# Performance work log

Measured on AMD Instinct MI355X. Metric: run time of the kernel, lower is better.

The kernel has to match this reference:

```python
import jax, jax.numpy as jnp
import numpy as np
import math

L, DIN, DZ, H, C, NQ, NP = 768, 384, 128, 12, 16, 4, 6
C_SQU = 1.0 / math.sqrt(C)            # scalar qk scale
W_C = math.sqrt(2.0 / (9 * NQ))       # point-distance scale


def _w(key, fan_in, fan_out):
    return jax.random.normal(key, (fan_in, fan_out), dtype=jnp.float32) / math.sqrt(fan_in)


def setup_inputs() -> dict:
    key = jax.random.key(0)
    ks = jax.random.split(key, 20)
    inp = {
        "s": jax.random.normal(ks[0], (L, DIN), dtype=jnp.float32),
        "z": jax.random.normal(ks[1], (L, L, DZ), dtype=jnp.float32),
        "rot": jax.random.normal(ks[2], (L, 3, 3), dtype=jnp.float32),
        "trans": jax.random.normal(ks[3], (L, 3), dtype=jnp.float32),
        "Wq1": _w(ks[4], DIN, H * C),
        "Wk1": _w(ks[5], DIN, H * C),
        "Wv1": _w(ks[6], DIN, H * C),
        "Wq2": _w(ks[7], DIN, H * NQ * 3),
        "Wk2": _w(ks[8], DIN, H * NQ * 3),
        "Wv3": _w(ks[9], DIN, H * NP * 3),
        "Wz": _w(ks[10], DZ, H),
        "W1": _w(ks[11], H * DZ, DIN),
        "b1": jnp.zeros((DIN,), dtype=jnp.float32),
        "W2": _w(ks[12], H * C, DIN),
        "b2": jnp.zeros((DIN,), dtype=jnp.float32),
        "W3": _w(ks[13], H * NP * 3, DIN),
        "b3": jnp.zeros((DIN,), dtype=jnp.float32),
        "gamma": jnp.zeros((H,), dtype=jnp.float32),
    }
    return inp


def ipa_transform(x, rot, trans):
    # x: [L,H,P,3] local points -> global: rot @ x + trans
    return jnp.einsum('lij,lhpj->lhpi', rot, x) + trans[:, None, None, :]


def ipa_inverse_transform(x, rot, trans):
    # global -> local: rot^T @ (x - trans)
    return jnp.einsum('lji,lhpj->lhpi', rot, x - trans[:, None, None, :])


def reference(s, z, rot, trans, Wq1, Wk1, Wv1, Wq2, Wk2, Wv3, Wz,
              W1, b1, W2, b2, W3, b3, gamma):
    q1 = (s @ Wq1).reshape(L, H, C)
    k1 = (s @ Wk1).reshape(L, H, C)
    v1 = (s @ Wv1).reshape(L, H, C)
    att = jnp.einsum('ihc,jhc->ijh', q1, k1) * C_SQU          # [L,L,H]
    bias_z = z @ Wz                                           # [L,L,H]
    q2 = ipa_transform((s @ Wq2).reshape(L, H, NQ, 3), rot, trans)
    k2 = ipa_transform((s @ Wk2).reshape(L, H, NQ, 3), rot, trans)
    # squared-distance map sum over query points & xyz, via |q|^2+|k|^2-2qk
    sq = jnp.sum(q2 * q2, axis=(-2, -1))                      # [L,H]
    sk = jnp.sum(k2 * k2, axis=(-2, -1))                      # [L,H]
    cross = jnp.einsum('ihqt,jhqt->ijh', q2, k2)              # [L,L,H]
    dismap = sq[:, None, :] + sk[None, :, :] - 2.0 * cross
    # NOTE: no softmax in the original module — raw scores weight the values.
    att = att + bias_z - jax.nn.softplus(gamma)[None, None, :] * dismap * (W_C * 0.5)
    o1 = jnp.einsum('ijh,ijd->ihd', att, z)                   # [L,H,DZ]
    o2 = jnp.einsum('jhc,ijh->ihc', v1, att)                  # [L,H,C]
    v3 = ipa_transform((s @ Wv3).reshape(L, H, NP, 3), rot, trans)
    o3 = ipa_inverse_transform(jnp.einsum('jhpt,ijh->ihpt', v3, att), rot, trans)
    out = (o1.reshape(L, -1) @ W1 + b1) \
        + (o2.reshape(L, -1) @ W2 + b2) \
        + (o3.reshape(L, -1) @ W3 + b3)
    return out
```

## Files before the change

### kernel.cpp

```cpp
#include <hip/hip_runtime.h>
#include <math.h>
#include <stdint.h>

#define LL 768
#define DIN 384
#define HH 12
#define NLIN 1080
#define WC_HALF 0.11785113019775792f
#define C_SQU 0.25f

#define OFF_LIN    0u
#define OFF_VT     829440u
#define OFF_QBH    1050624u
#define OFF_QBL    1198080u
#define OFF_KBH    1345536u
#define OFF_KBL    1492992u
#define OFF_WZ     1640448u
#define OFF_SQWH   1641472u
#define OFF_SKWH   1650688u
#define OFF_SX     1659904u
#define OFF_O2     8737792u
#define OFF_O3     8885248u
#define OFF_PO1    9051136u

typedef __attribute__((ext_vector_type(8))) short short8v;
typedef __attribute__((ext_vector_type(4))) float float4v;

__device__ __forceinline__ ushort f2bu(float f) {
    union { float f; uint32_t u; } v; v.f = f;
    uint32_t r = (v.u + 0x7FFFu + ((v.u >> 16) & 1u)) >> 16;
    return (ushort)r;
}
__device__ __forceinline__ float bu2f(ushort u) {
    union { uint32_t u; float f; } v; v.u = ((uint32_t)u) << 16; return v.f;
}
__device__ __forceinline__ int fswz(int j) {
    return (((j >> 3) << 1) | ((j >> 1) & 1)) << 4;
}

__global__ __launch_bounds__(256) void gemm_lin_kernel(
    const float* __restrict__ s,
    const float* __restrict__ Wq1, const float* __restrict__ Wk1,
    const float* __restrict__ Wv1, const float* __restrict__ Wq2,
    const float* __restrict__ Wk2, const float* __restrict__ Wv3,
    float* __restrict__ lin)
{
    const int n0 = blockIdx.x * 64;
    const int i0 = blockIdx.y * 64;
    const int tid = threadIdx.x;
    __shared__ float sT[64][17];
    __shared__ float wT[16][65];
    const int tc = tid & 15, tr = tid >> 4;
    float acc[4][4] = {};
    for (int k0 = 0; k0 < DIN; k0 += 16) {
        __syncthreads();
        for (int idx = tid; idx < 1024; idx += 256) {
            int r = idx >> 4, kk = idx & 15;
            sT[r][kk] = s[(size_t)(i0 + r) * DIN + k0 + kk];
        }
        for (int idx = tid; idx < 1024; idx += 256) {
            int kk = idx >> 6, c = idx & 63;
            int col = n0 + c;
            float v = 0.f;
            if (col < NLIN) {
                const float* W; int nout, cc2;
                if      (col < 192) { W = Wq1; nout = 192; cc2 = col; }
                else if (col < 384) { W = Wk1; nout = 192; cc2 = col - 192; }
                else if (col < 576) { W = Wv1; nout = 192; cc2 = col - 384; }
                else if (col < 720) { W = Wq2; nout = 144; cc2 = col - 576; }
                else if (col < 864) { W = Wk2; nout = 144; cc2 = col - 720; }
                else                { W = Wv3; nout = 216; cc2 = col - 864; }
                v = W[(size_t)(k0 + kk) * nout + cc2];
            }
            wT[kk][c] = v;
        }
        __syncthreads();
        #pragma unroll
        for (int kk = 0; kk < 16; ++kk) {
            float a[4], b[4];
            #pragma unroll
            for (int r = 0; r < 4; ++r) a[r] = sT[tr * 4 + r][kk];
            #pragma unroll
            for (int c = 0; c < 4; ++c) b[c] = wT[kk][tc * 4 + c];
            #pragma unroll
            for (int r = 0; r < 4; ++r)
                #pragma unroll
                for (int c = 0; c < 4; ++c) acc[r][c] += a[r] * b[c];
        }
    }
    for (int r = 0; r < 4; ++r)
        for (int c = 0; c < 4; ++c) {
            int col = n0 + tc * 4 + c;
            if (col < NLIN)
                lin[(size_t)(i0 + tr * 4 + r) * NLIN + col] = acc[r][c];
        }
}

__global__ __launch_bounds__(192) void transform_kernel(
    const float* __restrict__ lin, const float* __restrict__ rot,
    const float* __restrict__ trans, const float* __restrict__ gamma,
    const float* __restrict__ Wz,
    ushort* __restrict__ vT,
    ushort* __restrict__ qbh, ushort* __restrict__ qbl,
    ushort* __restrict__ kbh, ushort* __restrict__ kbl,
    ushort* __restrict__ wzpack,
    float* __restrict__ sqwh, float* __restrict__ skwh)
{
    const int l = blockIdx.x;
    const int tid = threadIdx.x;
    __shared__ float q2s[144], k2s[144], sqp[48], skp[48];
    __shared__ float v3s[216];
    __shared__ float whs[12];
    __shared__ float R[9], T[3];
    if (tid < 9) R[tid] = rot[l * 9 + tid];
    if (tid >= 9 && tid < 12) T[tid - 9] = trans[l * 3 + tid - 9];
    __syncthreads();
    if (tid < 48) {
        const float* x = &lin[(size_t)l * NLIN + 576 + tid * 3];
        float x0 = x[0], x1 = x[1], x2 = x[2], ss = 0.f;
        #pragma unroll
        for (int i2 = 0; i2 < 3; ++i2) {
            float v = R[i2*3+0]*x0 + R[i2*3+1]*x1 + R[i2*3+2]*x2 + T[i2];
            q2s[tid * 3 + i2] = v; ss += v * v;
        }
        sqp[tid] = ss;
    } else if (tid < 96) {
        int t2 = tid - 48;
        const float* x = &lin[(size_t)l * NLIN + 720 + t2 * 3];
        float x0 = x[0], x1 = x[1], x2 = x[2], ss = 0.f;
        #pragma unroll
        for (int i2 = 0; i2 < 3; ++i2) {
            float v = R[i2*3+0]*x0 + R[i2*3+1]*x1 + R[i2*3+2]*x2 + T[i2];
            k2s[t2 * 3 + i2] = v; ss += v * v;
        }
        skp[t2] = ss;
    } else if (tid < 168) {
        int t2 = tid - 96;
        const float* x = &lin[(size_t)l * NLIN + 864 + t2 * 3];
        float x0 = x[0], x1 = x[1], x2 = x[2];
        #pragma unroll
        for (int i2 = 0; i2 < 3; ++i2) {
            float v = R[i2*3+0]*x0 + R[i2*3+1]*x1 + R[i2*3+2]*x2 + T[i2];
            v3s[t2 * 3 + i2] = v;
        }
    }
    __syncthreads();
    if (tid < 12) {
        float sq = sqp[tid*4] + sqp[tid*4+1] + sqp[tid*4+2] + sqp[tid*4+3];
        float sk = skp[tid*4] + skp[tid*4+1] + skp[tid*4+2] + skp[tid*4+3];
        float w = logf(1.0f + expf(gamma[tid])) * WC_HALF;
        whs[tid] = w;
        sqwh[tid * 768 + l] = w * sq;
        skwh[tid * 768 + l] = w * sk;
    }
    __syncthreads();
    for (int w = tid; w < 408; w += 192) {
        int h = w / 34, c = w % 34;
        float v = (c < 16) ? lin[(size_t)l * NLIN + 384 + h * 16 + c]
                           : v3s[h * 18 + (c - 16)];
        vT[((size_t)h * 48 + c) * 768 + l] = f2bu(v);
    }
    for (int idx = tid; idx < 384; idx += 192) {
        int h = idx >> 5, k = idx & 31;
        float qv, kv;
        if (k < 16) {
            qv = lin[(size_t)l * NLIN + h * 16 + k];
            kv = C_SQU * lin[(size_t)l * NLIN + 192 + h * 16 + k];
        } else if (k < 28) {
            int u = k - 16;
            qv = q2s[h * 12 + u];
            kv = 2.0f * whs[h] * k2s[h * 12 + u];
        } else { qv = 0.0f; kv = 0.0f; }
        size_t base = ((size_t)h * 768 + l) * 32 + k;
        ushort qh = f2bu(qv), kh = f2bu(kv);
        qbh[base] = qh; qbl[base] = f2bu(qv - bu2f(qh));
        kbh[base] = kh; kbl[base] = f2bu(kv - bu2f(kh));
    }
    if (l == 0) {
        for (int idx = tid; idx < 2048; idx += 192) {
            int kb = idx >> 9, lane = (idx >> 3) & 63, e = idx & 7;
            int d = kb * 32 + (lane >> 4) * 8 + e, h = lane & 15;
            wzpack[idx] = (h < 12) ? f2bu(Wz[d * 12 + h]) : (ushort)0;
        }
    }
}

__global__ __launch_bounds__(256) void sextra_kernel(
    const ushort* __restrict__ qbh, const ushort* __restrict__ qbl,
    const ushort* __restrict__ kbh, const ushort* __restrict__ kbl,
    const float* __restrict__ sqwh, const float* __restrict__ skwh,
    float* __restrict__ sx)
{
    const int tid = threadIdx.x;
    const int wv = tid >> 6, lane = tid & 63, lm = lane & 15, g = lane >> 4;
    const int i0 = blockIdx.x * 16;
    const int jb = blockIdx.y * 64 + wv * 16;
    const int h = blockIdx.z;
    size_t qoff = ((size_t)h * 768 + i0 + lm) * 32 + g * 8;
    size_t koff = ((size_t)h * 768 + jb + lm) * 32 + g * 8;
    short8v ah = *(const short8v*)(qbh + qoff);
    short8v al = *(const short8v*)(qbl + qoff);
    short8v bh = *(const short8v*)(kbh + koff);
    short8v bl = *(const short8v*)(kbl + koff);
    float4v c1 = {0.f, 0.f, 0.f, 0.f};
    float4v c2 = {0.f, 0.f, 0.f, 0.f};
    c1 = __builtin_amdgcn_mfma_f32_16x16x32_bf16(ah, bh, c1, 0, 0, 0);
    c2 = __builtin_amdgcn_mfma_f32_16x16x32_bf16(ah, bl, c2, 0, 0, 0);
    c2 = __builtin_amdgcn_mfma_f32_16x16x32_bf16(al, bh, c2, 0, 0, 0);
    float skv = skwh[h * 768 + jb + lm];
    #pragma unroll
    for (int r = 0; r < 4; ++r) {
        int ii = i0 + g * 4 + r;
        sx[((size_t)ii * 12 + h) * 768 + jb + lm] =
            (c1[r] + c2[r]) - sqwh[h * 768 + ii] - skv;
    }
}

__global__ __launch_bounds__(256) void attn_kernel(
    const float* __restrict__ z, const ushort* __restrict__ wzp,
    float* sxa,
    float* __restrict__ po1)
{
    const int bid = blockIdx.x, tid = threadIdx.x;
    const int i = bid >> 1, t0 = (bid & 1) * 12;
    const int wv = tid >> 6, lane = tid & 63, lm = lane & 15, g = lane >> 4;
    __shared__ __attribute__((aligned(16))) char zrow[2][32 * 256];
    __shared__ __attribute__((aligned(16))) char attbh[16 * 80];
    __shared__ __attribute__((aligned(16))) char attbl[16 * 80];

    short8v wzf[4];
    #pragma unroll
    for (int kb = 0; kb < 4; ++kb)
        wzf[kb] = *(const short8v*)(wzp + (kb * 64 + lane) * 8);

    const float4* zsrc = (const float4*)(z + (size_t)i * (LL * 128));
    const int jA = wv * 16 + lm;

    {
        float4 z0[4];
        #pragma unroll
        for (int s = 0; s < 4; ++s) z0[s] = zsrc[(size_t)t0 * 1024 + s * 256 + tid];
        #pragma unroll
        for (int s = 0; s < 4; ++s) {
            int k4 = s * 256 + tid, j = k4 >> 5, d0 = (k4 & 31) * 4;
            float4 v = z0[s];
            ushort b0 = f2bu(v.x), b1 = f2bu(v.y), b2 = f2bu(v.z), b3 = f2bu(v.w);
            uint32_t lo = b0 | ((uint32_t)b1 << 16), hi = b2 | ((uint32_t)b3 << 16);
            *(uint64_t*)(&zrow[0][j * 256 + ((d0 * 2) ^ fswz(j))]) =
                (uint64_t)lo | ((uint64_t)hi << 32);
        }
    }
    float sxr[4] = {0.f, 0.f, 0.f, 0.f};
    if (wv < 2 && g < 3) {
        #pragma unroll
        for (int r = 0; r < 4; ++r)
            sxr[r] = sxa[((size_t)i * 12 + g * 4 + r) * 768 + t0 * 32 + jA];
    }
    __syncthreads();

    float4v acc1[2] = {{0.f,0.f,0.f,0.f}, {0.f,0.f,0.f,0.f}};
    int p = 0;

    for (int t = 0; t < 12; ++t) {
        const int tt = t0 + t, j0 = tt * 32;
        float4 zreg[4];
        if (t < 11) {
            #pragma unroll
            for (int s = 0; s < 4; ++s)
                zreg[s] = zsrc[(size_t)(tt + 1) * 1024 + s * 256 + tid];
        }
        float sxn[4] = {0.f, 0.f, 0.f, 0.f};
        if (wv < 2 && g < 3 && t < 11) {
            #pragma unroll
            for (int r = 0; r < 4; ++r)
                sxn[r] = sxa[((size_t)i * 12 + g * 4 + r) * 768 + j0 + 32 + jA];
        }
        if (wv < 2) {
            float4v bias = {0.f, 0.f, 0.f, 0.f};
            #pragma unroll
            for (int kb = 0; kb < 4; ++kb) {
                short8v bz = *(const short8v*)(
                    &zrow[p][jA * 256 + ((kb * 64 + g * 16) ^ fswz(jA))]);
                bias = __builtin_amdgcn_mfma_f32_16x16x32_bf16(wzf[kb], bz, bias, 0, 0, 0);
            }
            #pragma unroll
            for (int r = 0; r < 4; ++r) {
                int h = g * 4 + r;
                float att = bias[r] + sxr[r];
                ushort hi = f2bu(att);
                *(ushort*)(&attbh[h * 80 + jA * 2]) = hi;
                *(ushort*)(&attbl[h * 80 + jA * 2]) = f2bu(att - bu2f(hi));
                if (g < 3)
                    sxa[((size_t)i * 12 + h) * 768 + j0 + jA] = att;
            }
        }
        __syncthreads();
        {
            short8v ah = *(const short8v*)(&attbh[lm * 80 + g * 16]);
            short8v al = *(const short8v*)(&attbl[lm * 80 + g * 16]);
            #pragma unroll
            for (int q = 0; q < 2; ++q) {
                const int b = wv * 2 + q;
                short8v bf;
                #pragma unroll
                for (int e = 0; e < 8; ++e) {
                    int jj = g * 8 + e;
                    bf[e] = *(const short*)(&zrow[p][jj * 256 +
                              (((b * 16 + lm) * 2) ^ fswz(jj))]);
                }
                acc1[q] = __builtin_amdgcn_mfma_f32_16x16x32_bf16(ah, bf, acc1[q], 0, 0, 0);
                acc1[q] = __builtin_amdgcn_mfma_f32_16x16x32_bf16(al, bf, acc1[q], 0, 0, 0);
            }
        }
        if (t < 11) {
            #pragma unroll
            for (int s = 0; s < 4; ++s) {
                int k4 = s * 256 + tid, j = k4 >> 5, d0 = (k4 & 31) * 4;
                float4 v = zreg[s];
                ushort b0 = f2bu(v.x), b1 = f2bu(v.y), b2 = f2bu(v.z), b3 = f2bu(v.w);
                uint32_t lo = b0 | ((uint32_t)b1 << 16), hi = b2 | ((uint32_t)b3 << 16);
                *(uint64_t*)(&zrow[p ^ 1][j * 256 + ((d0 * 2) ^ fswz(j))]) =
                    (uint64_t)lo | ((uint64_t)hi << 32);
            }
        }
        __syncthreads();
        #pragma unroll
        for (int r = 0; r < 4; ++r) sxr[r] = sxn[r];
        p ^= 1;
    }
    if (g < 3) {
        #pragma unroll
        for (int q = 0; q < 2; ++q) {
            const int b = wv * 2 + q;
            #pragma unroll
            for (int r = 0; r < 4; ++r)
                po1[(size_t)bid * 1536 + (g * 4 + r) * 128 + b * 16 + lm] = acc1[q][r];
        }
    }
}

__global__ __launch_bounds__(64) void ov_kernel(
    const float* __restrict__ att, const ushort* __restrict__ vT,
    const float* __restrict__ rot, const float* __restrict__ trans,
    float* __restrict__ o2, float* __restrict__ o3l)
{
    const int i0 = blockIdx.x * 16;
    const int h = blockIdx.y;
    const int lane = threadIdx.x;
    const int lm = lane & 15, g = lane >> 4;
    __shared__ float o3s[16][18];

    float4v acc0 = {0.f,0.f,0.f,0.f};
    float4v acc1 = {0.f,0.f,0.f,0.f};
    float4v acc2 = {0.f,0.f,0.f,0.f};
    const float* arow = att + ((size_t)(i0 + lm) * 12 + h) * 768;
    const ushort* vbase = vT + (size_t)h * 48 * 768;
    for (int kt = 0; kt < 24; ++kt) {
        const float4* ap = (const float4*)(arow + kt * 32 + g * 8);
        float4 a0 = ap[0], a1 = ap[1];
        float av[8] = {a0.x, a0.y, a0.z, a0.w, a1.x, a1.y, a1.z, a1.w};
        short8v ah, al;
        #pragma unroll
        for (int e = 0; e < 8; ++e) {
            ushort hi = f2bu(av[e]);
            ah[e] = (short)hi;
            al[e] = (short)f2bu(av[e] - bu2f(hi));
        }
        const int kq = kt * 32 + g * 8;
        short8v b0 = *(const short8v*)(vbase + (size_t)(0 * 16 + lm) * 768 + kq);
        short8v b1 = *(const short8v*)(vbase + (size_t)(1 * 16 + lm) * 768 + kq);
        short8v b2 = *(const short8v*)(vbase + (size_t)(2 * 16 + lm) * 768 + kq);
        acc0 = __builtin_amdgcn_mfma_f32_16x16x32_bf16(ah, b0, acc0, 0, 0, 0);
        acc0 = __builtin_amdgcn_mfma_f32_16x16x32_bf16(al, b0, acc0, 0, 0, 0);
        acc1 = __builtin_amdgcn_mfma_f32_16x16x32_bf16(ah, b1, acc1, 0, 0, 0);
        acc1 = __builtin_amdgcn_mfma_f32_16x16x32_bf16(al, b1, acc1, 0, 0, 0);
        acc2 = __builtin_amdgcn_mfma_f32_16x16x32_bf16(ah, b2, acc2, 0, 0, 0);
        acc2 = __builtin_amdgcn_mfma_f32_16x16x32_bf16(al, b2, acc2, 0, 0, 0);
    }
    #pragma unroll
    for (int r = 0; r < 4; ++r)
        o2[(size_t)(i0 + g * 4 + r) * 192 + h * 16 + lm] = acc0[r];
    #pragma unroll
    for (int r = 0; r < 4; ++r) {
        int row = g * 4 + r;
        o3s[row][lm] = acc1[r];
        if (lm < 2) o3s[row][16 + lm] = acc2[r];
    }
    __syncthreads();
    for (int it = lane; it < 96; it += 64) {
        int row = it / 6, pp = it % 6;
        int ii = i0 + row;
        const float* R = &rot[(size_t)ii * 9];
        float x0 = o3s[row][pp * 3 + 0] - trans[ii * 3 + 0];
        float x1 = o3s[row][pp * 3 + 1] - trans[ii * 3 + 1];
        float x2 = o3s[row][pp * 3 + 2] - trans[ii * 3 + 2];
        o3l[(size_t)ii * 216 + h * 18 + pp * 3 + 0] = R[0]*x0 + R[3]*x1 + R[6]*x2;
        o3l[(size_t)ii * 216 + h * 18 + pp * 3 + 1] = R[1]*x0 + R[4]*x1 + R[7]*x2;
        o3l[(size_t)ii * 216 + h * 18 + pp * 3 + 2] = R[2]*x0 + R[5]*x1 + R[8]*x2;
    }
}

#define KCH 324
__global__ __launch_bounds__(384) void proj_kernel(
    const float* __restrict__ po1, const float* __restrict__ o2,
    const float* __restrict__ o3l,
    const float* __restrict__ W1, const float* __restrict__ W2,
    const float* __restrict__ W3,
    float* __restrict__ part)
{
    const int it = blockIdx.x, kt = blockIdx.y;
    const int tid = threadIdx.x;
    const int kbeg = kt * KCH, kend = kbeg + KCH;
    __shared__ float olds[16][KCH];
    for (int idx = tid; idx < 16 * KCH; idx += 384) {
        int r = idx / KCH, kk = idx % KCH;
        int k = kbeg + kk;
        int i = it * 16 + r;
        float v;
        if (k < 1536)
            v = po1[(size_t)(2 * i) * 1536 + k] + po1[(size_t)(2 * i + 1) * 1536 + k];
        else if (k < 1728)
            v = o2[(size_t)i * 192 + k - 1536];
        else
            v = o3l[(size_t)i * 216 + k - 1728];
        olds[r][kk] = v;
    }
    __syncthreads();
    float acc[16] = {};
    {
        int s0 = kbeg, s1 = (kend < 1536) ? kend : 1536;
        for (int k = s0; k < s1; ++k) {
            float w = W1[(size_t)k * 384 + tid];
            int kk = k - kbeg;
            #pragma unroll
            for (int r = 0; r < 16; ++r) acc[r] += olds[r][kk] * w;
        }
    }
    {
        int s0 = (kbeg > 1536) ? kbeg : 1536, s1 = (kend < 1728) ? kend : 1728;
        for (int k = s0; k < s1; ++k) {
            float w = W2[(size_t)(k - 1536) * 384 + tid];
            int kk = k - kbeg;
            #pragma unroll
            for (int r = 0; r < 16; ++r) acc[r] += olds[r][kk] * w;
        }
    }
    {
        int s0 = (kbeg > 1728) ? kbeg : 1728, s1 = kend;
        for (int k = s0; k < s1; ++k) {
            float w = W3[(size_t)(k - 1728) * 384 + tid];
            int kk = k - kbeg;
            #pragma unroll
            for (int r = 0; r < 16; ++r) acc[r] += olds[r][kk] * w;
        }
    }
    for (int r = 0; r < 16; ++r)
        part[((size_t)kt * LL + it * 16 + r) * 384 + tid] = acc[r];
}

__global__ __launch_bounds__(256) void final_kernel(
    const float* __restrict__ part,
    const float* __restrict__ b1, const float* __restrict__ b2,
    const float* __restrict__ b3, float* __restrict__ out)
{
    int idx = blockIdx.x * 256 + threadIdx.x;
    if (idx < LL * 384) {
        int n = idx % 384;
        float v = b1[n] + b2[n] + b3[n];
        #pragma unroll
        for (int kt = 0; kt < 6; ++kt) v += part[(size_t)kt * 294912 + idx];
        out[idx] = v;
    }
}

extern "C" void kernel_launch(void* const* d_in, const int* in_sizes, int n_in,
                              void* d_out, int out_size, void* d_ws, size_t ws_size,
                              hipStream_t stream) {
    const float* s     = (const float*)d_in[0];
    const float* z     = (const float*)d_in[1];
    const float* rot   = (const float*)d_in[2];
    const float* trans = (const float*)d_in[3];
    const float* Wq1   = (const float*)d_in[4];
    const float* Wk1   = (const float*)d_in[5];
    const float* Wv1   = (const float*)d_in[6];
    const float* Wq2   = (const float*)d_in[7];
    const float* Wk2   = (const float*)d_in[8];
    const float* Wv3   = (const float*)d_in[9];
    const float* Wz    = (const float*)d_in[10];
    const float* W1    = (const float*)d_in[11];
    const float* b1    = (const float*)d_in[12];
    const float* W2    = (const float*)d_in[13];
    const float* b2    = (const float*)d_in[14];
    const float* W3    = (const float*)d_in[15];
    const float* b3    = (const float*)d_in[16];
    const float* gamma = (const float*)d_in[17];
    float* ws  = (float*)d_ws;
    float* out = (float*)d_out;

    float*  lin  = ws + OFF_LIN;
    ushort* vT   = (ushort*)(ws + OFF_VT);
    ushort* qbh  = (ushort*)(ws + OFF_QBH);
    ushort* qbl  = (ushort*)(ws + OFF_QBL);
    ushort* kbh  = (ushort*)(ws + OFF_KBH);
    ushort* kbl  = (ushort*)(ws + OFF_KBL);
    ushort* wzp  = (ushort*)(ws + OFF_WZ);
    float*  sqwh = ws + OFF_SQWH;
    float*  skwh = ws + OFF_SKWH;
    float*  sx   = ws + OFF_SX;
    float*  o2   = ws + OFF_O2;
    float*  o3l  = ws + OFF_O3;
    float*  po1  = ws + OFF_PO1;
    float*  part = ws + OFF_SX;

    dim3 gA(17, 12);
    gemm_lin_kernel<<<gA, 256, 0, stream>>>(s, Wq1, Wk1, Wv1, Wq2, Wk2, Wv3, lin);
    transform_kernel<<<LL, 192, 0, stream>>>(lin, rot, trans, gamma, Wz,
                                             vT, qbh, qbl, kbh, kbl, wzp,
                                             sqwh, skwh);
    dim3 gS(48, 12, 12);
    sextra_kernel<<<gS, 256, 0, stream>>>(qbh, qbl, kbh, kbl, sqwh, skwh, sx);
    attn_kernel<<<LL * 2, 256, 0, stream>>>(z, wzp, sx, po1);
    dim3 gV(48, 12);
    ov_kernel<<<gV, 64, 0, stream>>>(sx, vT, rot, trans, o2, o3l);
    dim3 gC(48, 6);
    proj_kernel<<<gC, 384, 0, stream>>>(po1, o2, o3l, W1, W2, W3, part);
    final_kernel<<<(LL * 384 + 255) / 256, 256, 0, stream>>>(part, b1, b2, b3, out);
}
```

Before: 280.2 us.

## Split attention j-range four ways and parallelize ov_kernel across waves

attn_kernel now splits each row's j range into four chunks instead of two, which doubles the number of blocks. The next z tile is now converted to bf16 and written to shared memory before the MFMA stage rather than after it. ov_kernel uses 256 threads, and each of its four waves takes a strided share of the k-tiles. A shared-memory reduction then combines the four partial results, and proj_kernel sums four po1 partials per row. The aim is more parallelism and better occupancy on a memory-bound pass, at the cost of a partial buffer twice as large and extra reduction traffic.

```diff
diff --git a/kernel.cpp b/kernel.cpp
--- a/kernel.cpp
+++ b/kernel.cpp
@@ -222,7 +222,7 @@
     float* __restrict__ po1)
 {
     const int bid = blockIdx.x, tid = threadIdx.x;
-    const int i = bid >> 1, t0 = (bid & 1) * 12;
+    const int i = bid >> 2, t0 = (bid & 3) * 6;
     const int wv = tid >> 6, lane = tid & 63, lm = lane & 15, g = lane >> 4;
     __shared__ __attribute__((aligned(16))) char zrow[2][32 * 256];
     __shared__ __attribute__((aligned(16))) char attbh[16 * 80];
@@ -261,16 +261,16 @@
     float4v acc1[2] = {{0.f,0.f,0.f,0.f}, {0.f,0.f,0.f,0.f}};
     int p = 0;
 
-    for (int t = 0; t < 12; ++t) {
+    for (int t = 0; t < 6; ++t) {
         const int tt = t0 + t, j0 = tt * 32;
         float4 zreg[4];
-        if (t < 11) {
+        if (t < 5) {
             #pragma unroll
             for (int s = 0; s < 4; ++s)
                 zreg[s] = zsrc[(size_t)(tt + 1) * 1024 + s * 256 + tid];
         }
         float sxn[4] = {0.f, 0.f, 0.f, 0.f};
-        if (wv < 2 && g < 3 && t < 11) {
+        if (wv < 2 && g < 3 && t < 5) {
             #pragma unroll
             for (int r = 0; r < 4; ++r)
                 sxn[r] = sxa[((size_t)i * 12 + g * 4 + r) * 768 + j0 + 32 + jA];
@@ -295,6 +295,17 @@
             }
         }
         __syncthreads();
+        if (t < 5) {
+            #pragma unroll
+            for (int s = 0; s < 4; ++s) {
+                int k4 = s * 256 + tid, j = k4 >> 5, d0 = (k4 & 31) * 4;
+                float4 v = zreg[s];
+                ushort b0 = f2bu(v.x), b1 = f2bu(v.y), b2 = f2bu(v.z), b3 = f2bu(v.w);
+                uint32_t lo = b0 | ((uint32_t)b1 << 16), hi = b2 | ((uint32_t)b3 << 16);
+                *(uint64_t*)(&zrow[p ^ 1][j * 256 + ((d0 * 2) ^ fswz(j))]) =
+                    (uint64_t)lo | ((uint64_t)hi << 32);
+            }
+        }
         {
             short8v ah = *(const short8v*)(&attbh[lm * 80 + g * 16]);
             short8v al = *(const short8v*)(&attbl[lm * 80 + g * 16]);
@@ -312,17 +323,6 @@
                 acc1[q] = __builtin_amdgcn_mfma_f32_16x16x32_bf16(al, bf, acc1[q], 0, 0, 0);
             }
         }
-        if (t < 11) {
-            #pragma unroll
-            for (int s = 0; s < 4; ++s) {
-                int k4 = s * 256 + tid, j = k4 >> 5, d0 = (k4 & 31) * 4;
-                float4 v = zreg[s];
-                ushort b0 = f2bu(v.x), b1 = f2bu(v.y), b2 = f2bu(v.z), b3 = f2bu(v.w);
-                uint32_t lo = b0 | ((uint32_t)b1 << 16), hi = b2 | ((uint32_t)b3 << 16);
-                *(uint64_t*)(&zrow[p ^ 1][j * 256 + ((d0 * 2) ^ fswz(j))]) =
-                    (uint64_t)lo | ((uint64_t)hi << 32);
-            }
-        }
         __syncthreads();
         #pragma unroll
         for (int r = 0; r < 4; ++r) sxr[r] = sxn[r];
@@ -339,15 +339,17 @@
     }
 }
 
-__global__ __launch_bounds__(64) void ov_kernel(
+__global__ __launch_bounds__(256) void ov_kernel(
     const float* __restrict__ att, const ushort* __restrict__ vT,
     const float* __restrict__ rot, const float* __restrict__ trans,
     float* __restrict__ o2, float* __restrict__ o3l)
 {
     const int i0 = blockIdx.x * 16;
     const int h = blockIdx.y;
-    const int lane = threadIdx.x;
+    const int tid = threadIdx.x;
+    const int wv = tid >> 6, lane = tid & 63;
     const int lm = lane & 15, g = lane >> 4;
+    __shared__ float red[4][3][64][4];
     __shared__ float o3s[16][18];
 
     float4v acc0 = {0.f,0.f,0.f,0.f};
@@ -355,7 +357,7 @@
     float4v acc2 = {0.f,0.f,0.f,0.f};
     const float* arow = att + ((size_t)(i0 + lm) * 12 + h) * 768;
     const ushort* vbase = vT + (size_t)h * 48 * 768;
-    for (int kt = 0; kt < 24; ++kt) {
+    for (int kt = wv; kt < 24; kt += 4) {
         const float4* ap = (const float4*)(arow + kt * 32 + g * 8);
         float4 a0 = ap[0], a1 = ap[1];
         float av[8] = {a0.x, a0.y, a0.z, a0.w, a1.x, a1.y, a1.z, a1.w};
@@ -378,16 +380,25 @@
         acc2 = __builtin_amdgcn_mfma_f32_16x16x32_bf16(al, b2, acc2, 0, 0, 0);
     }
     #pragma unroll
-    for (int r = 0; r < 4; ++r)
-        o2[(size_t)(i0 + g * 4 + r) * 192 + h * 16 + lm] = acc0[r];
-    #pragma unroll
     for (int r = 0; r < 4; ++r) {
-        int row = g * 4 + r;
-        o3s[row][lm] = acc1[r];
-        if (lm < 2) o3s[row][16 + lm] = acc2[r];
-    }
-    __syncthreads();
-    for (int it = lane; it < 96; it += 64) {
+        red[wv][0][lane][r] = acc0[r];
+        red[wv][1][lane][r] = acc1[r];
+        red[wv][2][lane][r] = acc2[r];
+    }
+    __syncthreads();
+    for (int v = tid; v < 768; v += 256) {
+        int a = v >> 8, rem = v & 255;
+        int l2 = rem >> 2, r = rem & 3;
+        float sum = red[0][a][l2][r] + red[1][a][l2][r]
+                  + red[2][a][l2][r] + red[3][a][l2][r];
+        int lm2 = l2 & 15, g2 = l2 >> 4;
+        int row = g2 * 4 + r;
+        if (a == 0)      o2[(size_t)(i0 + row) * 192 + h * 16 + lm2] = sum;
+        else if (a == 1) o3s[row][lm2] = sum;
+        else if (lm2 < 2) o3s[row][16 + lm2] = sum;
+    }
+    __syncthreads();
+    for (int it = tid; it < 96; it += 256) {
         int row = it / 6, pp = it % 6;
         int ii = i0 + row;
         const float* R = &rot[(size_t)ii * 9];
@@ -418,7 +429,8 @@
         int i = it * 16 + r;
         float v;
         if (k < 1536)
-            v = po1[(size_t)(2 * i) * 1536 + k] + po1[(size_t)(2 * i + 1) * 1536 + k];
+            v = (po1[(size_t)(4 * i) * 1536 + k] + po1[(size_t)(4 * i + 1) * 1536 + k])
+              + (po1[(size_t)(4 * i + 2) * 1536 + k] + po1[(size_t)(4 * i + 3) * 1536 + k]);
         else if (k < 1728)
             v = o2[(size_t)i * 192 + k - 1536];
         else
@@ -519,9 +531,9 @@
                                              sqwh, skwh);
     dim3 gS(48, 12, 12);
     sextra_kernel<<<gS, 256, 0, stream>>>(qbh, qbl, kbh, kbl, sqwh, skwh, sx);
-    attn_kernel<<<LL * 2, 256, 0, stream>>>(z, wzp, sx, po1);
+    attn_kernel<<<LL * 4, 256, 0, stream>>>(z, wzp, sx, po1);
     dim3 gV(48, 12);
-    ov_kernel<<<gV, 64, 0, stream>>>(sx, vT, rot, trans, o2, o3l);
+    ov_kernel<<<gV, 256, 0, stream>>>(sx, vT, rot, trans, o2, o3l);
     dim3 gC(48, 6);
     proj_kernel<<<gC, 384, 0, stream>>>(po1, o2, o3l, W1, W2, W3, part);
     final_kernel<<<(LL * 384 + 255) / 256, 256, 0, stream>>>(part, b1, b2, b3, out);
```

After: 318.3 us. +13.6%, slower.

## Split fused attention kernel into separate bias and fp32 o1 kernels

Applied to the files above, without the earlier changes.

The fused attn_kernel, which computed the z bias and accumulated o1 with bf16 MFMA in one pass over z, is split into two kernels. bias_kernel computes the attention scores and writes them in two layouts (head-major and j-major). o1_kernel then rereads z in fp32 and accumulates o1 with scalar FMAs over 768 blocks of 128 threads. This reads the 302MB z tensor twice and drops tensor cores for o1, in exchange for fp32 precision on o1 and no split-row partial sums.

```diff
diff --git a/kernel.cpp b/kernel.cpp
--- a/kernel.cpp
+++ b/kernel.cpp
@@ -19,9 +19,12 @@
 #define OFF_SQWH   1641472u
 #define OFF_SKWH   1650688u
 #define OFF_SX     1659904u
-#define OFF_O2     8737792u
-#define OFF_O3     8885248u
-#define OFF_PO1    9051136u
+#define OFF_ATTH   8737792u
+#define OFF_ATTJ   15815680u
+#define OFF_O1     22893568u
+#define OFF_O2     24073216u
+#define OFF_O3     24220672u
+#define OFF_PART   24386560u
 
 typedef __attribute__((ext_vector_type(8))) short short8v;
 typedef __attribute__((ext_vector_type(4))) float float4v;
@@ -216,17 +219,15 @@
     }
 }
 
-__global__ __launch_bounds__(256) void attn_kernel(
+__global__ __launch_bounds__(256) void bias_kernel(
     const float* __restrict__ z, const ushort* __restrict__ wzp,
-    float* sxa,
-    float* __restrict__ po1)
-{
-    const int bid = blockIdx.x, tid = threadIdx.x;
-    const int i = bid >> 1, t0 = (bid & 1) * 12;
+    const float* __restrict__ sx,
+    float* __restrict__ attH, float* __restrict__ attJ)
+{
+    const int i = blockIdx.x, jt = blockIdx.y, j0 = jt * 32;
+    const int tid = threadIdx.x;
     const int wv = tid >> 6, lane = tid & 63, lm = lane & 15, g = lane >> 4;
-    __shared__ __attribute__((aligned(16))) char zrow[2][32 * 256];
-    __shared__ __attribute__((aligned(16))) char attbh[16 * 80];
-    __shared__ __attribute__((aligned(16))) char attbl[16 * 80];
+    __shared__ __attribute__((aligned(16))) char zrow[32 * 256];
 
     short8v wzf[4];
     #pragma unroll
@@ -234,109 +235,93 @@
         wzf[kb] = *(const short8v*)(wzp + (kb * 64 + lane) * 8);
 
     const float4* zsrc = (const float4*)(z + (size_t)i * (LL * 128));
-    const int jA = wv * 16 + lm;
-
     {
         float4 z0[4];
         #pragma unroll
-        for (int s = 0; s < 4; ++s) z0[s] = zsrc[(size_t)t0 * 1024 + s * 256 + tid];
+        for (int s = 0; s < 4; ++s) z0[s] = zsrc[(size_t)jt * 1024 + s * 256 + tid];
         #pragma unroll
         for (int s = 0; s < 4; ++s) {
             int k4 = s * 256 + tid, j = k4 >> 5, d0 = (k4 & 31) * 4;
             float4 v = z0[s];
             ushort b0 = f2bu(v.x), b1 = f2bu(v.y), b2 = f2bu(v.z), b3 = f2bu(v.w);
             uint32_t lo = b0 | ((uint32_t)b1 << 16), hi = b2 | ((uint32_t)b3 << 16);
-            *(uint64_t*)(&zrow[0][j * 256 + ((d0 * 2) ^ fswz(j))]) =
+            *(uint64_t*)(&zrow[j * 256 + ((d0 * 2) ^ fswz(j))]) =
                 (uint64_t)lo | ((uint64_t)hi << 32);
         }
     }
-    float sxr[4] = {0.f, 0.f, 0.f, 0.f};
-    if (wv < 2 && g < 3) {
-        #pragma unroll
-        for (int r = 0; r < 4; ++r)
-            sxr[r] = sxa[((size_t)i * 12 + g * 4 + r) * 768 + t0 * 32 + jA];
-    }
     __syncthreads();
-
-    float4v acc1[2] = {{0.f,0.f,0.f,0.f}, {0.f,0.f,0.f,0.f}};
-    int p = 0;
-
-    for (int t = 0; t < 12; ++t) {
-        const int tt = t0 + t, j0 = tt * 32;
-        float4 zreg[4];
-        if (t < 11) {
-            #pragma unroll
-            for (int s = 0; s < 4; ++s)
-                zreg[s] = zsrc[(size_t)(tt + 1) * 1024 + s * 256 + tid];
-        }
-        float sxn[4] = {0.f, 0.f, 0.f, 0.f};
-        if (wv < 2 && g < 3 && t < 11) {
-            #pragma unroll
-            for (int r = 0; r < 4; ++r)
-                sxn[r] = sxa[((size_t)i * 12 + g * 4 + r) * 768 + j0 + 32 + jA];
-        }
-        if (wv < 2) {
-            float4v bias = {0.f, 0.f, 0.f, 0.f};
-            #pragma unroll
-            for (int kb = 0; kb < 4; ++kb) {
-                short8v bz = *(const short8v*)(
-                    &zrow[p][jA * 256 + ((kb * 64 + g * 16) ^ fswz(jA))]);
-                bias = __builtin_amdgcn_mfma_f32_16x16x32_bf16(wzf[kb], bz, bias, 0, 0, 0);
-            }
+    if (wv < 2) {
+        const int jA = wv * 16 + lm;
+        float4v bias = {0.f, 0.f, 0.f, 0.f};
+        #pragma unroll
+        for (int kb = 0; kb < 4; ++kb) {
+            short8v bz = *(const short8v*)(
+                &zrow[jA * 256 + ((kb * 64 + g * 16) ^ fswz(jA))]);
+            bias = __builtin_amdgcn_mfma_f32_16x16x32_bf16(wzf[kb], bz, bias, 0, 0, 0);
+        }
+        if (g < 3) {
             #pragma unroll
             for (int r = 0; r < 4; ++r) {
                 int h = g * 4 + r;
-                float att = bias[r] + sxr[r];
-                ushort hi = f2bu(att);
-                *(ushort*)(&attbh[h * 80 + jA * 2]) = hi;
-                *(ushort*)(&attbl[h * 80 + jA * 2]) = f2bu(att - bu2f(hi));
-                if (g < 3)
-                    sxa[((size_t)i * 12 + h) * 768 + j0 + jA] = att;
+                float att = bias[r] + sx[((size_t)i * 12 + h) * 768 + j0 + jA];
+                attH[((size_t)i * 12 + h) * 768 + j0 + jA] = att;
+                attJ[((size_t)i * 768 + j0 + jA) * 12 + h] = att;
             }
         }
-        __syncthreads();
-        {
-            short8v ah = *(const short8v*)(&attbh[lm * 80 + g * 16]);
-            short8v al = *(const short8v*)(&attbl[lm * 80 + g * 16]);
-            #pragma unroll
-            for (int q = 0; q < 2; ++q) {
-                const int b = wv * 2 + q;
-                short8v bf;
-                #pragma unroll
-                for (int e = 0; e < 8; ++e) {
-                    int jj = g * 8 + e;
-                    bf[e] = *(const short*)(&zrow[p][jj * 256 +
-                              (((b * 16 + lm) * 2) ^ fswz(jj))]);
-                }
-                acc1[q] = __builtin_amdgcn_mfma_f32_16x16x32_bf16(ah, bf, acc1[q], 0, 0, 0);
-                acc1[q] = __builtin_amdgcn_mfma_f32_16x16x32_bf16(al, bf, acc1[q], 0, 0, 0);
-            }
-        }
-        if (t < 11) {
-            #pragma unroll
-            for (int s = 0; s < 4; ++s) {
-                int k4 = s * 256 + tid, j = k4 >> 5, d0 = (k4 & 31) * 4;
-                float4 v = zreg[s];
-                ushort b0 = f2bu(v.x), b1 = f2bu(v.y), b2 = f2bu(v.z), b3 = f2bu(v.w);
-                uint32_t lo = b0 | ((uint32_t)b1 << 16), hi = b2 | ((uint32_t)b3 << 16);
-                *(uint64_t*)(&zrow[p ^ 1][j * 256 + ((d0 * 2) ^ fswz(j))]) =
-                    (uint64_t)lo | ((uint64_t)hi << 32);
-            }
-        }
-        __syncthreads();
-        #pragma unroll
-        for (int r = 0; r < 4; ++r) sxr[r] = sxn[r];
-        p ^= 1;
-    }
-    if (g < 3) {
-        #pragma unroll
-        for (int q = 0; q < 2; ++q) {
-            const int b = wv * 2 + q;
-            #pragma unroll
-            for (int r = 0; r < 4; ++r)
-                po1[(size_t)bid * 1536 + (g * 4 + r) * 128 + b * 16 + lm] = acc1[q][r];
-        }
-    }
+    }
+}
+
+__global__ __launch_bounds__(128) void o1_kernel(
+    const float* __restrict__ z, const float* __restrict__ attJ,
+    float* __restrict__ o1)
+{
+    const int i = blockIdx.x, d = threadIdx.x;
+    const float* zb = z + (size_t)i * (LL * 128);
+    const float* ab = attJ + (size_t)i * (LL * 12);
+    float acc[12] = {};
+    float za[32], zb2[32];
+
+    #pragma unroll
+    for (int jj = 0; jj < 32; ++jj) za[jj] = zb[(size_t)jj * 128 + d];
+
+    #pragma unroll 1
+    for (int jt = 0; jt < 24; jt += 2) {
+        #pragma unroll
+        for (int jj = 0; jj < 32; ++jj)
+            zb2[jj] = zb[(size_t)((jt + 1) * 32 + jj) * 128 + d];
+        #pragma unroll
+        for (int jj = 0; jj < 32; ++jj) {
+            const float4* ar = (const float4*)(ab + (size_t)(jt * 32 + jj) * 12);
+            float4 a0 = ar[0], a1 = ar[1], a2 = ar[2];
+            float zv = za[jj];
+            acc[0] += a0.x * zv; acc[1] += a0.y * zv;
+            acc[2] += a0.z * zv; acc[3] += a0.w * zv;
+            acc[4] += a1.x * zv; acc[5] += a1.y * zv;
+            acc[6] += a1.z * zv; acc[7] += a1.w * zv;
+            acc[8] += a2.x * zv; acc[9] += a2.y * zv;
+            acc[10] += a2.z * zv; acc[11] += a2.w * zv;
+        }
+        if (jt + 2 < 24) {
+            #pragma unroll
+            for (int jj = 0; jj < 32; ++jj)
+                za[jj] = zb[(size_t)((jt + 2) * 32 + jj) * 128 + d];
+        }
+        #pragma unroll
+        for (int jj = 0; jj < 32; ++jj) {
+            const float4* ar = (const float4*)(ab + (size_t)((jt + 1) * 32 + jj) * 12);
+            float4 a0 = ar[0], a1 = ar[1], a2 = ar[2];
+            float zv = zb2[jj];
+            acc[0] += a0.x * zv; acc[1] += a0.y * zv;
+            acc[2] += a0.z * zv; acc[3] += a0.w * zv;
+            acc[4] += a1.x * zv; acc[5] += a1.y * zv;
+            acc[6] += a1.z * zv; acc[7] += a1.w * zv;
+            acc[8] += a2.x * zv; acc[9] += a2.y * zv;
+            acc[10] += a2.z * zv; acc[11] += a2.w * zv;
+        }
+    }
+    #pragma unroll
+    for (int h = 0; h < 12; ++h)
+        o1[(size_t)i * 1536 + h * 128 + d] = acc[h];
 }
 
 __global__ __launch_bounds__(64) void ov_kernel(
@@ -402,7 +387,7 @@
 
 #define KCH 324
 __global__ __launch_bounds__(384) void proj_kernel(
-    const float* __restrict__ po1, const float* __restrict__ o2,
+    const float* __restrict__ o1, const float* __restrict__ o2,
     const float* __restrict__ o3l,
     const float* __restrict__ W1, const float* __restrict__ W2,
     const float* __restrict__ W3,
@@ -417,12 +402,9 @@
         int k = kbeg + kk;
         int i = it * 16 + r;
         float v;
-        if (k < 1536)
-            v = po1[(size_t)(2 * i) * 1536 + k] + po1[(size_t)(2 * i + 1) * 1536 + k];
-        else if (k < 1728)
-            v = o2[(size_t)i * 192 + k - 1536];
-        else
-            v = o3l[(size_t)i * 216 + k - 1728];
+        if (k < 1536)      v = o1[(size_t)i * 1536 + k];
+        else if (k < 1728) v = o2[(size_t)i * 192 + k - 1536];
+        else               v = o3l[(size_t)i * 216 + k - 1728];
         olds[r][kk] = v;
     }
     __syncthreads();
@@ -507,10 +489,12 @@
     float*  sqwh = ws + OFF_SQWH;
     float*  skwh = ws + OFF_SKWH;
     float*  sx   = ws + OFF_SX;
+    float*  attH = ws + OFF_ATTH;
+    float*  attJ = ws + OFF_ATTJ;
+    float*  o1   = ws + OFF_O1;
     float*  o2   = ws + OFF_O2;
     float*  o3l  = ws + OFF_O3;
-    float*  po1  = ws + OFF_PO1;
-    float*  part = ws + OFF_SX;
+    float*  part = ws + OFF_PART;
 
     dim3 gA(17, 12);
     gemm_lin_kernel<<<gA, 256, 0, stream>>>(s, Wq1, Wk1, Wv1, Wq2, Wk2, Wv3, lin);
@@ -519,10 +503,12 @@
                                              sqwh, skwh);
     dim3 gS(48, 12, 12);
     sextra_kernel<<<gS, 256, 0, stream>>>(qbh, qbl, kbh, kbl, sqwh, skwh, sx);
-    attn_kernel<<<LL * 2, 256, 0, stream>>>(z, wzp, sx, po1);
+    dim3 gB(LL, 24);
+    bias_kernel<<<gB, 256, 0, stream>>>(z, wzp, sx, attH, attJ);
+    o1_kernel<<<LL, 128, 0, stream>>>(z, attJ, o1);
     dim3 gV(48, 12);
-    ov_kernel<<<gV, 64, 0, stream>>>(sx, vT, rot, trans, o2, o3l);
+    ov_kernel<<<gV, 64, 0, stream>>>(attH, vT, rot, trans, o2, o3l);
     dim3 gC(48, 6);
-    proj_kernel<<<gC, 384, 0, stream>>>(po1, o2, o3l, W1, W2, W3, part);
+    proj_kernel<<<gC, 384, 0, stream>>>(o1, o2, o3l, W1, W2, W3, part);
     final_kernel<<<(LL * 384 + 255) / 256, 256, 0, stream>>>(part, b1, b2, b3, out);
 }
```

After: 508.9 us. 81.6% more time.
